# Performance work log

Hardware: AMD Instinct MI355X
Metric: run time of the kernel (lower is better)

The kernel has to match this reference:

```python
import jax, jax.numpy as jnp
import numpy as np
import math

B, T, C, H = 2, 2048, 1024, 16
HD = C // H  # head dim = 64

def setup_inputs() -> dict:
    key = jax.random.key(0)
    ks = jax.random.split(key, 5)
    s = 1.0 / math.sqrt(C)
    return {
        "x": jax.random.normal(ks[0], (B, T, C), jnp.float32),
        "Wq": jax.random.normal(ks[1], (C, C), jnp.float32) * s,
        "bq": jnp.zeros((C,), jnp.float32),
        "Wk": jax.random.normal(ks[2], (C, C), jnp.float32) * s,
        "bk": jnp.zeros((C,), jnp.float32),
        "Wv": jax.random.normal(ks[3], (C, C), jnp.float32) * s,
        "bv": jnp.zeros((C,), jnp.float32),
        "Wp": jax.random.normal(ks[4], (C, C), jnp.float32) * s,
        "bp": jnp.zeros((C,), jnp.float32),
    }

def reference(x, Wq, bq, Wk, bk, Wv, bv, Wp, bp):
    # project and split heads: [B,T,C] -> [B,H,T,HD]
    def heads(y):
        return y.reshape(B, T, H, HD).transpose(0, 2, 1, 3)
    q = heads(x @ Wq + bq)
    k = heads(x @ Wk + bk)
    v = heads(x @ Wv + bv)
    scale = 1.0 / math.sqrt(HD)
    att = jnp.einsum('bhqd,bhkd->bhqk', q, k) * scale  # [B,H,T,T]
    causal = jnp.tril(jnp.ones((T, T), bool))
    att = jnp.where(causal, att, -jnp.inf)
    att = jax.nn.softmax(att, axis=-1)  # attention_dropout p=0 -> identity
    y = jnp.einsum('bhqk,bhkd->bhqd', att, v)  # [B,H,T,HD]
    y = y.transpose(0, 2, 1, 3).reshape(B, T, C)
    return y @ Wp + bp  # residual_dropout p=0 -> identity
```

## Files before the change

### kernel.cpp

```cpp
#include <hip/hip_runtime.h>
#include <hip/hip_bf16.h>
#include <stdint.h>

typedef __bf16 bf16x8 __attribute__((ext_vector_type(8)));
typedef __bf16 bf16x4 __attribute__((ext_vector_type(4)));
typedef float  f32x4  __attribute__((ext_vector_type(4)));

#define MFMA16(a, b, c) __builtin_amdgcn_mfma_f32_16x16x32_bf16(a, b, c, 0, 0, 0)

#if __has_builtin(__builtin_amdgcn_exp2f)
#define EXP2(x) __builtin_amdgcn_exp2f(x)
#else
#define EXP2(x) exp2f(x)
#endif

__device__ __forceinline__ void ld16(void* lds, const void* g) {
    __builtin_amdgcn_global_load_lds(
        (const __attribute__((address_space(1))) void*)(uintptr_t)g,
        (__attribute__((address_space(3))) void*)(uint32_t)(uintptr_t)lds,
        16, 0, 0);
}

__global__ __launch_bounds__(1024) void prep_kernel(const float* __restrict__ x,
                                                    const float* __restrict__ W0,
                                                    const float* __restrict__ W1,
                                                    const float* __restrict__ W2,
                                                    const float* __restrict__ W3,
                                                    __bf16* __restrict__ wdst,
                                                    __bf16* __restrict__ xdst) {
    __shared__ __bf16 t[32][33];
    const int z = blockIdx.z;
    const int tx = threadIdx.x, ty = threadIdx.y;
    if (z == 4) {
        int blin = blockIdx.y * 32 + blockIdx.x;
        int i = (blin * 1024 + ty * 32 + tx) * 4;
        float4 v = *(const float4*)(x + i);
        xdst[i]     = (__bf16)v.x;
        xdst[i + 1] = (__bf16)v.y;
        xdst[i + 2] = (__bf16)v.z;
        xdst[i + 3] = (__bf16)v.w;
        return;
    }
    const float* W = (z == 0) ? W0 : (z == 1) ? W1 : (z == 2) ? W2 : W3;
    __bf16* D = wdst + (size_t)z * 1048576;
    t[ty][tx] = (__bf16)W[(size_t)(blockIdx.y * 32 + ty) * 1024 + blockIdx.x * 32 + tx];
    __syncthreads();
    D[(size_t)(blockIdx.x * 32 + ty) * 1024 + blockIdx.y * 32 + tx] = t[tx][ty];
}

__device__ __forceinline__ void gemm_mainloop(const __bf16* __restrict__ A,
                                              const __bf16* __restrict__ BT,
                                              int K, __bf16* As, __bf16* Bs,
                                              f32x4 acc[4][4]) {
    const int tid  = threadIdx.x;
    const int lane = tid & 63;
    const int wid  = tid >> 6;
    const int quad = lane >> 4;
    const int l16  = lane & 15;
    const int wm   = wid >> 1;
    const int wn   = wid & 1;

    const int srow = wid * 16 + (lane >> 2);
    const int scol = (lane & 3) * 8;
    const int sdst = wid * 512 + lane * 8;

    for (int k0 = 0; k0 < K; k0 += 32) {
        ld16(As + sdst,        A  + (size_t)srow        * K + k0 + scol);
        ld16(As + 2048 + sdst, A  + (size_t)(srow + 64) * K + k0 + scol);
        ld16(Bs + sdst,        BT + (size_t)srow        * K + k0 + scol);
        ld16(Bs + 2048 + sdst, BT + (size_t)(srow + 64) * K + k0 + scol);
        __syncthreads();
        bf16x8 af[4], bf[4];
#pragma unroll
        for (int mt = 0; mt < 4; mt++)
            af[mt] = *(const bf16x8*)(As + (wm * 64 + mt * 16 + l16) * 32 + quad * 8);
#pragma unroll
        for (int nt = 0; nt < 4; nt++)
            bf[nt] = *(const bf16x8*)(Bs + (wn * 64 + nt * 16 + l16) * 32 + quad * 8);
#pragma unroll
        for (int mt = 0; mt < 4; mt++)
#pragma unroll
            for (int nt = 0; nt < 4; nt++)
                acc[mt][nt] = MFMA16(af[mt], bf[nt], acc[mt][nt]);
        __syncthreads();
    }
}

__global__ __launch_bounds__(256) void qkv_gemm(const __bf16* __restrict__ X,
                                                const __bf16* __restrict__ WTb,
                                                const float* __restrict__ b0,
                                                const float* __restrict__ b1,
                                                const float* __restrict__ b2,
                                                __bf16* __restrict__ qk,
                                                __bf16* __restrict__ vt) {
    __shared__ __attribute__((aligned(16))) __bf16 As[4096];
    __shared__ __attribute__((aligned(16))) __bf16 Bs[4096];
    const int o  = blockIdx.x;
    const int g  = o & 7, r = o >> 3;
    const int mB = ((g >> 1) << 3) + (r & 7);
    const int nz = (g & 1) * 12 + (r >> 3);
    const int z  = nz >> 3;
    const int n  = nz & 7;
    const __bf16* BT   = WTb + (size_t)z * 1048576;
    const float* bias  = (z == 0) ? b0 : (z == 1) ? b1 : b2;
    const int m0 = mB * 128, n0 = n * 128;
    f32x4 acc[4][4];
    const f32x4 zz = {0.f, 0.f, 0.f, 0.f};
#pragma unroll
    for (int i = 0; i < 4; i++)
#pragma unroll
        for (int j = 0; j < 4; j++) acc[i][j] = zz;
    gemm_mainloop(X + (size_t)m0 * 1024, BT + (size_t)n0 * 1024, 1024, As, Bs, acc);

    const int lane = threadIdx.x & 63, wid = threadIdx.x >> 6;
    const int quad = lane >> 4, l16 = lane & 15, wm = wid >> 1, wn = wid & 1;
    if (z == 2) {
#pragma unroll
        for (int nt = 0; nt < 4; nt++) {
            int col = n0 + wn * 64 + nt * 16 + l16;
            float bv = bias[col];
            int h = col >> 6, hd = col & 63;
#pragma unroll
            for (int mt = 0; mt < 4; mt++) {
                int m = m0 + wm * 64 + mt * 16 + quad * 4;
                int b = m >> 11, tt = m & 2047;
                bf16x4 pk;
                pk.x = (__bf16)(acc[mt][nt].x + bv);
                pk.y = (__bf16)(acc[mt][nt].y + bv);
                pk.z = (__bf16)(acc[mt][nt].z + bv);
                pk.w = (__bf16)(acc[mt][nt].w + bv);
                *(bf16x4*)(vt + ((size_t)((b * 16 + h) * 64 + hd)) * 2048 + tt) = pk;
            }
        }
    } else {
        const float sq = (z == 0) ? 0.18033688011112042f : 1.0f;
        __bf16* dst = qk + (size_t)z * 4194304;
#pragma unroll
        for (int nt = 0; nt < 4; nt++) {
            int col = n0 + wn * 64 + nt * 16 + l16;
            float bv = bias[col];
            int h = col >> 6, hd = col & 63;
#pragma unroll
            for (int mt = 0; mt < 4; mt++) {
#pragma unroll
                for (int r4 = 0; r4 < 4; r4++) {
                    int m = m0 + wm * 64 + mt * 16 + quad * 4 + r4;
                    int b = m >> 11, tt = m & 2047;
                    float v = (acc[mt][nt][r4] + bv) * sq;
                    dst[((size_t)((b * 16 + h) * 2048 + tt)) * 64 + hd] = (__bf16)v;
                }
            }
        }
    }
}

__global__ __launch_bounds__(256) void proj_gemm(const __bf16* __restrict__ Yw,
                                                 const __bf16* __restrict__ WT,
                                                 const float* __restrict__ bias,
                                                 float* __restrict__ out) {
    __shared__ __attribute__((aligned(16))) __bf16 As[4096];
    __shared__ __attribute__((aligned(16))) __bf16 Bs[4096];
    const int o = blockIdx.x;
    const int g = o & 7, r = o >> 3;
    const int m0 = (g * 4 + (r & 3)) * 128;
    const int n0 = (r >> 2) * 128;
    f32x4 acc[4][4];
    const f32x4 zz = {0.f, 0.f, 0.f, 0.f};
#pragma unroll
    for (int i = 0; i < 4; i++)
#pragma unroll
        for (int j = 0; j < 4; j++) acc[i][j] = zz;
    gemm_mainloop(Yw + (size_t)m0 * 1024, WT + (size_t)n0 * 1024, 1024, As, Bs, acc);

    const int lane = threadIdx.x & 63, wid = threadIdx.x >> 6;
    const int quad = lane >> 4, l16 = lane & 15, wm = wid >> 1, wn = wid & 1;
#pragma unroll
    for (int nt = 0; nt < 4; nt++) {
        int col = n0 + wn * 64 + nt * 16 + l16;
        float bv = bias[col];
#pragma unroll
        for (int mt = 0; mt < 4; mt++) {
#pragma unroll
            for (int r4 = 0; r4 < 4; r4++) {
                int m = m0 + wm * 64 + mt * 16 + quad * 4 + r4;
                out[(size_t)m * 1024 + col] = acc[mt][nt][r4] + bv;
            }
        }
    }
}

__global__ __launch_bounds__(512, 1) void attn_kernel(const __bf16* __restrict__ Qg,
                                                      const __bf16* __restrict__ Kg,
                                                      const __bf16* __restrict__ Vtg,
                                                      __bf16* __restrict__ Y) {
    __shared__ __attribute__((aligned(16))) __bf16 Kb[2][128 * 64];
    __shared__ __attribute__((aligned(16))) __bf16 Vb[2][64 * 128];
    __shared__ __attribute__((aligned(16))) __bf16 Ps[8][16 * 136];
    __shared__ __attribute__((aligned(16))) float  Lw[8][16];

    const int tid  = threadIdx.x;
    const int lane = tid & 63;
    const int wid  = tid >> 6;
    const int quad = lane >> 4;
    const int l16  = lane & 15;
    const int bkid = blockIdx.x;
    const int head  = ((bkid & 7) << 2) + ((bkid >> 3) & 3);
    const int ipair = bkid >> 5;
    const size_t hbase = (size_t)head * (2048 * 64);
    const f32x4 zz = {0.f, 0.f, 0.f, 0.f};

    const int kr  = lane >> 3;
    const int kc8 = (lane & 7) ^ kr;
    const int vr  = lane >> 4;
    const int vl  = lane & 15;

#pragma unroll 1
    for (int itm = 0; itm < 2; itm++) {
        const int qi  = itm ? (15 - ipair) : ipair;
        const int ktl = qi;
        const int q0  = qi << 7;
        const int q0w = q0 + wid * 16;

        bf16x8 qf[2];
#pragma unroll
        for (int kk = 0; kk < 2; kk++)
            qf[kk] = *(const bf16x8*)(Qg + hbase +
                                      (size_t)(q0w + l16) * 64 + kk * 32 + quad * 8);

        f32x4 acc_o[4];
#pragma unroll
        for (int jj = 0; jj < 4; jj++) acc_o[jj] = zz;
        float l_s = 0.f;

        auto stage = [&](int bf, int key0) {
#pragma unroll
            for (int i = 0; i < 2; i++) {
                const int c = wid * 2 + i;
                ld16((char*)&Kb[bf][0] + c * 1024 + lane * 16,
                     Kg + hbase + (size_t)(key0 + c * 8 + kr) * 64 + kc8 * 8);
            }
#pragma unroll
            for (int i = 0; i < 2; i++) {
                const int c = wid * 2 + i;
                const int row = c * 4 + vr;
                const int vc  = vl ^ (row & 7);
                ld16((char*)&Vb[bf][0] + c * 1024 + lane * 16,
                     Vtg + hbase + (size_t)row * 2048 + key0 + vc * 8);
            }
        };

        stage(0, 0);
        __syncthreads();
        int buf = 0;

#pragma unroll 1
        for (int kt = 0; kt <= ktl; kt++) {
            if (kt < ktl) stage(buf ^ 1, (kt + 1) << 7);

            f32x4 accs[8];
#pragma unroll
            for (int mt = 0; mt < 8; mt++) accs[mt] = zz;
#pragma unroll
            for (int kk = 0; kk < 2; kk++) {
#pragma unroll
                for (int mt = 0; mt < 8; mt++) {
                    bf16x8 kf = *(const bf16x8*)(&Kb[buf][(mt * 16 + l16) * 64 +
                                                 (((kk * 4 + quad) ^ (l16 & 7)) << 3)]);
                    accs[mt] = MFMA16(kf, qf[kk], accs[mt]);
                }
            }

            if (kt == ktl) {
#pragma unroll
                for (int mt = 0; mt < 8; mt++) {
                    int q_g = wid * 16 + l16;
#pragma unroll
                    for (int r4 = 0; r4 < 4; r4++) {
                        int key_g = mt * 16 + quad * 4 + r4;
                        if (key_g > q_g) accs[mt][r4] = -1e30f;
                    }
                }
            }

            float s_s = 0.f;
#pragma unroll
            for (int mt = 0; mt < 8; mt++) {
                f32x4 pv;
                pv.x = EXP2(accs[mt].x);
                pv.y = EXP2(accs[mt].y);
                pv.z = EXP2(accs[mt].z);
                pv.w = EXP2(accs[mt].w);
                s_s += (pv.x + pv.y) + (pv.z + pv.w);
                bf16x4 pk;
                pk.x = (__bf16)pv.x; pk.y = (__bf16)pv.y;
                pk.z = (__bf16)pv.z; pk.w = (__bf16)pv.w;
                *(bf16x4*)(&Ps[wid][l16 * 136 + mt * 16 + quad * 4]) = pk;
            }
            {
                float t = s_s;
                t += __shfl_xor(t, 16);
                t += __shfl_xor(t, 32);
                l_s += t;
            }

#pragma unroll
            for (int kk = 0; kk < 4; kk++) {
                bf16x8 pf, vf[4];
                pf = *(const bf16x8*)(&Ps[wid][l16 * 136 + kk * 32 + quad * 8]);
#pragma unroll
                for (int nv = 0; nv < 4; nv++)
                    vf[nv] = *(const bf16x8*)(&Vb[buf][(nv * 16 + l16) * 128 +
                                              (((kk * 4 + quad) ^ (l16 & 7)) << 3)]);
#pragma unroll
                for (int nv = 0; nv < 4; nv++)
                    acc_o[nv] = MFMA16(pf, vf[nv], acc_o[nv]);
            }

            __syncthreads();
            buf ^= 1;
        }

        if (quad == 0) Lw[wid][l16] = l_s;
        float* Om = (float*)&Ps[wid][0];
#pragma unroll
        for (int nv = 0; nv < 4; nv++)
#pragma unroll
            for (int r4 = 0; r4 < 4; r4++)
                Om[(quad * 4 + r4) * 68 + nv * 16 + l16] = acc_o[nv][r4];
        __syncthreads();

        {
            const int q  = lane >> 2;
            const int d0 = (lane & 3) * 16;
            float li = 1.0f / Lw[wid][q];
            f32x4 s0 = *(const f32x4*)(&Om[q * 68 + d0]);
            f32x4 s1 = *(const f32x4*)(&Om[q * 68 + d0 + 4]);
            f32x4 s2 = *(const f32x4*)(&Om[q * 68 + d0 + 8]);
            f32x4 s3 = *(const f32x4*)(&Om[q * 68 + d0 + 12]);
            bf16x8 o0, o1;
            o0[0] = (__bf16)(s0.x * li); o0[1] = (__bf16)(s0.y * li);
            o0[2] = (__bf16)(s0.z * li); o0[3] = (__bf16)(s0.w * li);
            o0[4] = (__bf16)(s1.x * li); o0[5] = (__bf16)(s1.y * li);
            o0[6] = (__bf16)(s1.z * li); o0[7] = (__bf16)(s1.w * li);
            o1[0] = (__bf16)(s2.x * li); o1[1] = (__bf16)(s2.y * li);
            o1[2] = (__bf16)(s2.z * li); o1[3] = (__bf16)(s2.w * li);
            o1[4] = (__bf16)(s3.x * li); o1[5] = (__bf16)(s3.y * li);
            o1[6] = (__bf16)(s3.z * li); o1[7] = (__bf16)(s3.w * li);
            const int bb = head >> 4, hh = head & 15;
            __bf16* yp = Y + ((size_t)(bb * 2048 + q0w + q)) * 1024 + hh * 64 + d0;
            *(bf16x8*)(yp)     = o0;
            *(bf16x8*)(yp + 8) = o1;
        }
        __syncthreads();
    }
}

#define XB_OFF  0
#define WT_OFF  4194304
#define Q_OFF   8388608
#define K_OFF   12582912
#define VT_OFF  16777216
#define Y_OFF   0

extern "C" void kernel_launch(void* const* d_in, const int* in_sizes, int n_in,
                              void* d_out, int out_size, void* d_ws, size_t ws_size,
                              hipStream_t stream) {
    const float* x  = (const float*)d_in[0];
    const float* Wq = (const float*)d_in[1];
    const float* bq = (const float*)d_in[2];
    const float* Wk = (const float*)d_in[3];
    const float* bk = (const float*)d_in[4];
    const float* Wv = (const float*)d_in[5];
    const float* bv = (const float*)d_in[6];
    const float* Wp = (const float*)d_in[7];
    const float* bp = (const float*)d_in[8];
    __bf16* ws  = (__bf16*)d_ws;
    float*  out = (float*)d_out;
    if (ws_size < (size_t)41943040) return;

    prep_kernel<<<dim3(32, 32, 5), dim3(32, 32), 0, stream>>>(x, Wq, Wk, Wv, Wp,
                                                              ws + WT_OFF, ws + XB_OFF);
    qkv_gemm<<<dim3(768), 256, 0, stream>>>(ws + XB_OFF, ws + WT_OFF, bq, bk, bv,
                                            ws + Q_OFF, ws + VT_OFF);
    attn_kernel<<<dim3(256), 512, 0, stream>>>(ws + Q_OFF, ws + K_OFF, ws + VT_OFF,
                                               ws + Y_OFF);
    proj_gemm<<<dim3(256), 256, 0, stream>>>(ws + Y_OFF, ws + WT_OFF + 3 * 1048576, bp, out);
}
```

Baseline: 177.3 us.

## Widen GEMM K-tile to 64 with XOR-swizzled LDS and add MFMA priority hints

New measurement: 189.8 us. 1.07x slower.

```diff
diff --git a/kernel.cpp b/kernel.cpp
--- a/kernel.cpp
+++ b/kernel.cpp
@@ -60,28 +60,37 @@
     const int wm   = wid >> 1;
     const int wn   = wid & 1;
 
-    const int srow = wid * 16 + (lane >> 2);
-    const int scol = (lane & 3) * 8;
-    const int sdst = wid * 512 + lane * 8;
-
-    for (int k0 = 0; k0 < K; k0 += 32) {
-        ld16(As + sdst,        A  + (size_t)srow        * K + k0 + scol);
-        ld16(As + 2048 + sdst, A  + (size_t)(srow + 64) * K + k0 + scol);
-        ld16(Bs + sdst,        BT + (size_t)srow        * K + k0 + scol);
-        ld16(Bs + 2048 + sdst, BT + (size_t)(srow + 64) * K + k0 + scol);
+    const int lr = lane >> 3;
+    const int lc = (lane & 7) ^ lr;
+    const int l8 = l16 & 7;
+
+    for (int k0 = 0; k0 < K; k0 += 64) {
+#pragma unroll
+        for (int i = 0; i < 4; i++) {
+            const int r0 = wid * 32 + i * 8;
+            ld16((char*)As + r0 * 128 + lane * 16,
+                 A  + (size_t)(r0 + lr) * K + k0 + lc * 8);
+            ld16((char*)Bs + r0 * 128 + lane * 16,
+                 BT + (size_t)(r0 + lr) * K + k0 + lc * 8);
+        }
         __syncthreads();
-        bf16x8 af[4], bf[4];
-#pragma unroll
-        for (int mt = 0; mt < 4; mt++)
-            af[mt] = *(const bf16x8*)(As + (wm * 64 + mt * 16 + l16) * 32 + quad * 8);
-#pragma unroll
-        for (int nt = 0; nt < 4; nt++)
-            bf[nt] = *(const bf16x8*)(Bs + (wn * 64 + nt * 16 + l16) * 32 + quad * 8);
-#pragma unroll
-        for (int mt = 0; mt < 4; mt++)
+#pragma unroll
+        for (int kk = 0; kk < 2; kk++) {
+            bf16x8 af[4], bf[4];
+#pragma unroll
+            for (int mt = 0; mt < 4; mt++)
+                af[mt] = *(const bf16x8*)(As + (wm * 64 + mt * 16 + l16) * 64 +
+                                          (((kk * 4 + quad) ^ l8) << 3));
 #pragma unroll
             for (int nt = 0; nt < 4; nt++)
-                acc[mt][nt] = MFMA16(af[mt], bf[nt], acc[mt][nt]);
+                bf[nt] = *(const bf16x8*)(Bs + (wn * 64 + nt * 16 + l16) * 64 +
+                                          (((kk * 4 + quad) ^ l8) << 3));
+#pragma unroll
+            for (int mt = 0; mt < 4; mt++)
+#pragma unroll
+                for (int nt = 0; nt < 4; nt++)
+                    acc[mt][nt] = MFMA16(af[mt], bf[nt], acc[mt][nt]);
+        }
         __syncthreads();
     }
 }
@@ -93,8 +102,8 @@
                                                 const float* __restrict__ b2,
                                                 __bf16* __restrict__ qk,
                                                 __bf16* __restrict__ vt) {
-    __shared__ __attribute__((aligned(16))) __bf16 As[4096];
-    __shared__ __attribute__((aligned(16))) __bf16 Bs[4096];
+    __shared__ __attribute__((aligned(16))) __bf16 As[8192];
+    __shared__ __attribute__((aligned(16))) __bf16 Bs[8192];
     const int o  = blockIdx.x;
     const int g  = o & 7, r = o >> 3;
     const int mB = ((g >> 1) << 3) + (r & 7);
@@ -158,8 +167,8 @@
                                                  const __bf16* __restrict__ WT,
                                                  const float* __restrict__ bias,
                                                  float* __restrict__ out) {
-    __shared__ __attribute__((aligned(16))) __bf16 As[4096];
-    __shared__ __attribute__((aligned(16))) __bf16 Bs[4096];
+    __shared__ __attribute__((aligned(16))) __bf16 As[8192];
+    __shared__ __attribute__((aligned(16))) __bf16 Bs[8192];
     const int o = blockIdx.x;
     const int g = o & 7, r = o >> 3;
     const int m0 = (g * 4 + (r & 3)) * 128;
@@ -260,6 +269,7 @@
             f32x4 accs[8];
 #pragma unroll
             for (int mt = 0; mt < 8; mt++) accs[mt] = zz;
+            __builtin_amdgcn_s_setprio(1);
 #pragma unroll
             for (int kk = 0; kk < 2; kk++) {
 #pragma unroll
@@ -269,6 +279,7 @@
                     accs[mt] = MFMA16(kf, qf[kk], accs[mt]);
                 }
             }
+            __builtin_amdgcn_s_setprio(0);
 
             if (kt == ktl) {
 #pragma unroll
@@ -311,9 +322,11 @@
                 for (int nv = 0; nv < 4; nv++)
                     vf[nv] = *(const bf16x8*)(&Vb[buf][(nv * 16 + l16) * 128 +
                                               (((kk * 4 + quad) ^ (l16 & 7)) << 3)]);
+                __builtin_amdgcn_s_setprio(1);
 #pragma unroll
                 for (int nv = 0; nv < 4; nv++)
                     acc_o[nv] = MFMA16(pf, vf[nv], acc_o[nv]);
+                __builtin_amdgcn_s_setprio(0);
             }
 
             __syncthreads();
```

## Fuse prep, QKV GEMM, attention and projection into one persistent kernel

Applied to the files above, without the earlier changes.

Measured after the change: 278.3 us. 57.0% more time.

```diff
diff --git a/kernel.cpp b/kernel.cpp
--- a/kernel.cpp
+++ b/kernel.cpp
@@ -21,64 +21,51 @@
         16, 0, 0);
 }
 
-__global__ __launch_bounds__(1024) void prep_kernel(const float* __restrict__ x,
-                                                    const float* __restrict__ W0,
-                                                    const float* __restrict__ W1,
-                                                    const float* __restrict__ W2,
-                                                    const float* __restrict__ W3,
-                                                    __bf16* __restrict__ wdst,
-                                                    __bf16* __restrict__ xdst) {
-    __shared__ __bf16 t[32][33];
-    const int z = blockIdx.z;
-    const int tx = threadIdx.x, ty = threadIdx.y;
-    if (z == 4) {
-        int blin = blockIdx.y * 32 + blockIdx.x;
-        int i = (blin * 1024 + ty * 32 + tx) * 4;
-        float4 v = *(const float4*)(x + i);
-        xdst[i]     = (__bf16)v.x;
-        xdst[i + 1] = (__bf16)v.y;
-        xdst[i + 2] = (__bf16)v.z;
-        xdst[i + 3] = (__bf16)v.w;
-        return;
-    }
-    const float* W = (z == 0) ? W0 : (z == 1) ? W1 : (z == 2) ? W2 : W3;
-    __bf16* D = wdst + (size_t)z * 1048576;
-    t[ty][tx] = (__bf16)W[(size_t)(blockIdx.y * 32 + ty) * 1024 + blockIdx.x * 32 + tx];
+#define XB_OFF  0
+#define WT_OFF  4194304
+#define Q_OFF   8388608
+#define K_OFF   12582912
+#define VT_OFF  16777216
+#define Y_OFF   0
+
+__device__ __forceinline__ void gsync(unsigned* bar) {
     __syncthreads();
-    D[(size_t)(blockIdx.x * 32 + ty) * 1024 + blockIdx.y * 32 + tx] = t[tx][ty];
-}
-
-__device__ __forceinline__ void gemm_mainloop(const __bf16* __restrict__ A,
-                                              const __bf16* __restrict__ BT,
-                                              int K, __bf16* As, __bf16* Bs,
-                                              f32x4 acc[4][4]) {
+    if (threadIdx.x == 0) {
+        __threadfence();
+        atomicAdd(bar, 1u);
+        while (atomicAdd(bar, 0u) < 256u) { __builtin_amdgcn_s_sleep(8); }
+        __threadfence();
+    }
+    __syncthreads();
+}
+
+__device__ __forceinline__ void mainloop512(const __bf16* __restrict__ A,
+                                            const __bf16* __restrict__ BT,
+                                            __bf16* As, __bf16* Bs,
+                                            f32x4 acc[2][4]) {
     const int tid  = threadIdx.x;
     const int lane = tid & 63;
-    const int wid  = tid >> 6;
     const int quad = lane >> 4;
     const int l16  = lane & 15;
+    const int wid  = tid >> 6;
     const int wm   = wid >> 1;
     const int wn   = wid & 1;
-
-    const int srow = wid * 16 + (lane >> 2);
-    const int scol = (lane & 3) * 8;
-    const int sdst = wid * 512 + lane * 8;
-
-    for (int k0 = 0; k0 < K; k0 += 32) {
-        ld16(As + sdst,        A  + (size_t)srow        * K + k0 + scol);
-        ld16(As + 2048 + sdst, A  + (size_t)(srow + 64) * K + k0 + scol);
-        ld16(Bs + sdst,        BT + (size_t)srow        * K + k0 + scol);
-        ld16(Bs + 2048 + sdst, BT + (size_t)(srow + 64) * K + k0 + scol);
+    const int srow = tid >> 2;
+    const int scol = (tid & 3) * 8;
+
+    for (int k0 = 0; k0 < 1024; k0 += 32) {
+        ld16(As + tid * 8, A  + (size_t)srow * 1024 + k0 + scol);
+        ld16(Bs + tid * 8, BT + (size_t)srow * 1024 + k0 + scol);
         __syncthreads();
-        bf16x8 af[4], bf[4];
-#pragma unroll
-        for (int mt = 0; mt < 4; mt++)
-            af[mt] = *(const bf16x8*)(As + (wm * 64 + mt * 16 + l16) * 32 + quad * 8);
+        bf16x8 af[2], bf[4];
+#pragma unroll
+        for (int mt = 0; mt < 2; mt++)
+            af[mt] = *(const bf16x8*)(As + (wm * 32 + mt * 16 + l16) * 32 + quad * 8);
 #pragma unroll
         for (int nt = 0; nt < 4; nt++)
             bf[nt] = *(const bf16x8*)(Bs + (wn * 64 + nt * 16 + l16) * 32 + quad * 8);
 #pragma unroll
-        for (int mt = 0; mt < 4; mt++)
+        for (int mt = 0; mt < 2; mt++)
 #pragma unroll
             for (int nt = 0; nt < 4; nt++)
                 acc[mt][nt] = MFMA16(af[mt], bf[nt], acc[mt][nt]);
@@ -86,117 +73,14 @@
     }
 }
 
-__global__ __launch_bounds__(256) void qkv_gemm(const __bf16* __restrict__ X,
-                                                const __bf16* __restrict__ WTb,
-                                                const float* __restrict__ b0,
-                                                const float* __restrict__ b1,
-                                                const float* __restrict__ b2,
-                                                __bf16* __restrict__ qk,
-                                                __bf16* __restrict__ vt) {
-    __shared__ __attribute__((aligned(16))) __bf16 As[4096];
-    __shared__ __attribute__((aligned(16))) __bf16 Bs[4096];
-    const int o  = blockIdx.x;
-    const int g  = o & 7, r = o >> 3;
-    const int mB = ((g >> 1) << 3) + (r & 7);
-    const int nz = (g & 1) * 12 + (r >> 3);
-    const int z  = nz >> 3;
-    const int n  = nz & 7;
-    const __bf16* BT   = WTb + (size_t)z * 1048576;
-    const float* bias  = (z == 0) ? b0 : (z == 1) ? b1 : b2;
-    const int m0 = mB * 128, n0 = n * 128;
-    f32x4 acc[4][4];
-    const f32x4 zz = {0.f, 0.f, 0.f, 0.f};
-#pragma unroll
-    for (int i = 0; i < 4; i++)
-#pragma unroll
-        for (int j = 0; j < 4; j++) acc[i][j] = zz;
-    gemm_mainloop(X + (size_t)m0 * 1024, BT + (size_t)n0 * 1024, 1024, As, Bs, acc);
-
-    const int lane = threadIdx.x & 63, wid = threadIdx.x >> 6;
-    const int quad = lane >> 4, l16 = lane & 15, wm = wid >> 1, wn = wid & 1;
-    if (z == 2) {
-#pragma unroll
-        for (int nt = 0; nt < 4; nt++) {
-            int col = n0 + wn * 64 + nt * 16 + l16;
-            float bv = bias[col];
-            int h = col >> 6, hd = col & 63;
-#pragma unroll
-            for (int mt = 0; mt < 4; mt++) {
-                int m = m0 + wm * 64 + mt * 16 + quad * 4;
-                int b = m >> 11, tt = m & 2047;
-                bf16x4 pk;
-                pk.x = (__bf16)(acc[mt][nt].x + bv);
-                pk.y = (__bf16)(acc[mt][nt].y + bv);
-                pk.z = (__bf16)(acc[mt][nt].z + bv);
-                pk.w = (__bf16)(acc[mt][nt].w + bv);
-                *(bf16x4*)(vt + ((size_t)((b * 16 + h) * 64 + hd)) * 2048 + tt) = pk;
-            }
-        }
-    } else {
-        const float sq = (z == 0) ? 0.18033688011112042f : 1.0f;
-        __bf16* dst = qk + (size_t)z * 4194304;
-#pragma unroll
-        for (int nt = 0; nt < 4; nt++) {
-            int col = n0 + wn * 64 + nt * 16 + l16;
-            float bv = bias[col];
-            int h = col >> 6, hd = col & 63;
-#pragma unroll
-            for (int mt = 0; mt < 4; mt++) {
-#pragma unroll
-                for (int r4 = 0; r4 < 4; r4++) {
-                    int m = m0 + wm * 64 + mt * 16 + quad * 4 + r4;
-                    int b = m >> 11, tt = m & 2047;
-                    float v = (acc[mt][nt][r4] + bv) * sq;
-                    dst[((size_t)((b * 16 + h) * 2048 + tt)) * 64 + hd] = (__bf16)v;
-                }
-            }
-        }
-    }
-}
-
-__global__ __launch_bounds__(256) void proj_gemm(const __bf16* __restrict__ Yw,
-                                                 const __bf16* __restrict__ WT,
-                                                 const float* __restrict__ bias,
-                                                 float* __restrict__ out) {
-    __shared__ __attribute__((aligned(16))) __bf16 As[4096];
-    __shared__ __attribute__((aligned(16))) __bf16 Bs[4096];
-    const int o = blockIdx.x;
-    const int g = o & 7, r = o >> 3;
-    const int m0 = (g * 4 + (r & 3)) * 128;
-    const int n0 = (r >> 2) * 128;
-    f32x4 acc[4][4];
-    const f32x4 zz = {0.f, 0.f, 0.f, 0.f};
-#pragma unroll
-    for (int i = 0; i < 4; i++)
-#pragma unroll
-        for (int j = 0; j < 4; j++) acc[i][j] = zz;
-    gemm_mainloop(Yw + (size_t)m0 * 1024, WT + (size_t)n0 * 1024, 1024, As, Bs, acc);
-
-    const int lane = threadIdx.x & 63, wid = threadIdx.x >> 6;
-    const int quad = lane >> 4, l16 = lane & 15, wm = wid >> 1, wn = wid & 1;
-#pragma unroll
-    for (int nt = 0; nt < 4; nt++) {
-        int col = n0 + wn * 64 + nt * 16 + l16;
-        float bv = bias[col];
-#pragma unroll
-        for (int mt = 0; mt < 4; mt++) {
-#pragma unroll
-            for (int r4 = 0; r4 < 4; r4++) {
-                int m = m0 + wm * 64 + mt * 16 + quad * 4 + r4;
-                out[(size_t)m * 1024 + col] = acc[mt][nt][r4] + bv;
-            }
-        }
-    }
-}
-
-__global__ __launch_bounds__(512, 1) void attn_kernel(const __bf16* __restrict__ Qg,
-                                                      const __bf16* __restrict__ Kg,
-                                                      const __bf16* __restrict__ Vtg,
-                                                      __bf16* __restrict__ Y) {
-    __shared__ __attribute__((aligned(16))) __bf16 Kb[2][128 * 64];
-    __shared__ __attribute__((aligned(16))) __bf16 Vb[2][64 * 128];
-    __shared__ __attribute__((aligned(16))) __bf16 Ps[8][16 * 136];
-    __shared__ __attribute__((aligned(16))) float  Lw[8][16];
+__global__ __launch_bounds__(512, 1) void mega_kernel(
+        const float* __restrict__ x,
+        const float* __restrict__ Wq, const float* __restrict__ bq,
+        const float* __restrict__ Wk, const float* __restrict__ bk,
+        const float* __restrict__ Wv, const float* __restrict__ bv,
+        const float* __restrict__ Wp, const float* __restrict__ bp,
+        __bf16* ws, float* out, unsigned* bar) {
+    __shared__ __attribute__((aligned(16))) char smem[100864];
 
     const int tid  = threadIdx.x;
     const int lane = tid & 63;
@@ -204,163 +88,293 @@
     const int quad = lane >> 4;
     const int l16  = lane & 15;
     const int bkid = blockIdx.x;
-    const int head  = ((bkid & 7) << 2) + ((bkid >> 3) & 3);
-    const int ipair = bkid >> 5;
-    const size_t hbase = (size_t)head * (2048 * 64);
     const f32x4 zz = {0.f, 0.f, 0.f, 0.f};
 
-    const int kr  = lane >> 3;
-    const int kc8 = (lane & 7) ^ kr;
-    const int vr  = lane >> 4;
-    const int vl  = lane & 15;
+    {
+        __bf16* xb = ws + XB_OFF;
+        const int gtid = bkid * 512 + tid;
+#pragma unroll
+        for (int j = 0; j < 8; j++) {
+            int i = (gtid + j * 131072) * 4;
+            float4 v = *(const float4*)(x + i);
+            xb[i]     = (__bf16)v.x;
+            xb[i + 1] = (__bf16)v.y;
+            xb[i + 2] = (__bf16)v.z;
+            xb[i + 3] = (__bf16)v.w;
+        }
+        __bf16 (*t)[33] = (__bf16(*)[33])smem;
+        const int tx = tid & 31, ty = tid >> 5;
+        for (int tt = 0; tt < 16; tt++) {
+            const int tile = bkid * 16 + tt;
+            const int z = tile >> 10, rem = tile & 1023;
+            const int by = rem >> 5, bx = rem & 31;
+            const float* W = (z == 0) ? Wq : (z == 1) ? Wk : (z == 2) ? Wv : Wp;
+            __bf16* D = ws + WT_OFF + (size_t)z * 1048576;
+            t[ty][tx]      = (__bf16)W[(size_t)(by * 32 + ty) * 1024 + bx * 32 + tx];
+            t[ty + 16][tx] = (__bf16)W[(size_t)(by * 32 + ty + 16) * 1024 + bx * 32 + tx];
+            __syncthreads();
+            D[(size_t)(bx * 32 + ty) * 1024 + by * 32 + tx]      = t[tx][ty];
+            D[(size_t)(bx * 32 + ty + 16) * 1024 + by * 32 + tx] = t[tx][ty + 16];
+            __syncthreads();
+        }
+    }
+    gsync(&bar[0]);
+
+    {
+        __bf16* As = (__bf16*)smem;
+        __bf16* Bs = As + 4096;
+        const int g = bkid & 7, r0 = bkid >> 3;
+        const int wm = wid >> 1, wn = wid & 1;
+        for (int t3 = 0; t3 < 3; t3++) {
+            const int r  = r0 + t3 * 32;
+            const int mB = ((g >> 1) << 3) + (r & 7);
+            const int nz = (g & 1) * 12 + (r >> 3);
+            const int z  = nz >> 3;
+            const int n  = nz & 7;
+            const int m0 = mB * 128, n0 = n * 128;
+            const __bf16* BT  = ws + WT_OFF + (size_t)z * 1048576;
+            const float* bias = (z == 0) ? bq : (z == 1) ? bk : bv;
+            f32x4 acc[2][4];
+#pragma unroll
+            for (int i = 0; i < 2; i++)
+#pragma unroll
+                for (int j = 0; j < 4; j++) acc[i][j] = zz;
+            mainloop512(ws + XB_OFF + (size_t)m0 * 1024, BT + (size_t)n0 * 1024,
+                        As, Bs, acc);
+            if (z == 2) {
+                __bf16* vt = ws + VT_OFF;
+#pragma unroll
+                for (int nt = 0; nt < 4; nt++) {
+                    int col = n0 + wn * 64 + nt * 16 + l16;
+                    float bv = bias[col];
+                    int h = col >> 6, hd = col & 63;
+#pragma unroll
+                    for (int mt = 0; mt < 2; mt++) {
+                        int m = m0 + wm * 32 + mt * 16 + quad * 4;
+                        int b = m >> 11, tt = m & 2047;
+                        bf16x4 pk;
+                        pk.x = (__bf16)(acc[mt][nt].x + bv);
+                        pk.y = (__bf16)(acc[mt][nt].y + bv);
+                        pk.z = (__bf16)(acc[mt][nt].z + bv);
+                        pk.w = (__bf16)(acc[mt][nt].w + bv);
+                        *(bf16x4*)(vt + ((size_t)((b * 16 + h) * 64 + hd)) * 2048 + tt) = pk;
+                    }
+                }
+            } else {
+                const float sq = (z == 0) ? 0.18033688011112042f : 1.0f;
+                __bf16* dst = ws + Q_OFF + (size_t)z * 4194304;
+#pragma unroll
+                for (int nt = 0; nt < 4; nt++) {
+                    int col = n0 + wn * 64 + nt * 16 + l16;
+                    float bv = bias[col];
+                    int h = col >> 6, hd = col & 63;
+#pragma unroll
+                    for (int mt = 0; mt < 2; mt++) {
+#pragma unroll
+                        for (int r4 = 0; r4 < 4; r4++) {
+                            int m = m0 + wm * 32 + mt * 16 + quad * 4 + r4;
+                            int b = m >> 11, tt = m & 2047;
+                            float v = (acc[mt][nt][r4] + bv) * sq;
+                            dst[((size_t)((b * 16 + h) * 2048 + tt)) * 64 + hd] = (__bf16)v;
+                        }
+                    }
+                }
+            }
+        }
+    }
+    gsync(&bar[1]);
+
+    {
+        __bf16 (*Kb)[128 * 64] = (__bf16(*)[128 * 64])(smem);
+        __bf16 (*Vb)[64 * 128] = (__bf16(*)[64 * 128])(smem + 32768);
+        __bf16 (*Ps)[16 * 136] = (__bf16(*)[16 * 136])(smem + 65536);
+        float  (*Lw)[16]       = (float(*)[16])(smem + 100352);
+        const __bf16* Qg  = ws + Q_OFF;
+        const __bf16* Kg  = ws + K_OFF;
+        const __bf16* Vtg = ws + VT_OFF;
+        __bf16* Y = ws + Y_OFF;
+
+        const int head  = ((bkid & 7) << 2) + ((bkid >> 3) & 3);
+        const int ipair = bkid >> 5;
+        const size_t hbase = (size_t)head * (2048 * 64);
+
+        const int kr  = lane >> 3;
+        const int kc8 = (lane & 7) ^ kr;
+        const int vr  = lane >> 4;
+        const int vl  = lane & 15;
 
 #pragma unroll 1
-    for (int itm = 0; itm < 2; itm++) {
-        const int qi  = itm ? (15 - ipair) : ipair;
-        const int ktl = qi;
-        const int q0  = qi << 7;
-        const int q0w = q0 + wid * 16;
-
-        bf16x8 qf[2];
-#pragma unroll
-        for (int kk = 0; kk < 2; kk++)
-            qf[kk] = *(const bf16x8*)(Qg + hbase +
-                                      (size_t)(q0w + l16) * 64 + kk * 32 + quad * 8);
-
-        f32x4 acc_o[4];
-#pragma unroll
-        for (int jj = 0; jj < 4; jj++) acc_o[jj] = zz;
-        float l_s = 0.f;
-
-        auto stage = [&](int bf, int key0) {
-#pragma unroll
-            for (int i = 0; i < 2; i++) {
-                const int c = wid * 2 + i;
-                ld16((char*)&Kb[bf][0] + c * 1024 + lane * 16,
-                     Kg + hbase + (size_t)(key0 + c * 8 + kr) * 64 + kc8 * 8);
+        for (int itm = 0; itm < 2; itm++) {
+            const int qi  = itm ? (15 - ipair) : ipair;
+            const int ktl = qi;
+            const int q0  = qi << 7;
+            const int q0w = q0 + wid * 16;
+
+            bf16x8 qf[2];
+#pragma unroll
+            for (int kk = 0; kk < 2; kk++)
+                qf[kk] = *(const bf16x8*)(Qg + hbase +
+                                          (size_t)(q0w + l16) * 64 + kk * 32 + quad * 8);
+
+            f32x4 acc_o[4];
+#pragma unroll
+            for (int jj = 0; jj < 4; jj++) acc_o[jj] = zz;
+            float l_s = 0.f;
+
+            auto stage = [&](int bf, int key0) {
+#pragma unroll
+                for (int i = 0; i < 2; i++) {
+                    const int c = wid * 2 + i;
+                    ld16((char*)&Kb[bf][0] + c * 1024 + lane * 16,
+                         Kg + hbase + (size_t)(key0 + c * 8 + kr) * 64 + kc8 * 8);
+                }
+#pragma unroll
+                for (int i = 0; i < 2; i++) {
+                    const int c = wid * 2 + i;
+                    const int row = c * 4 + vr;
+                    const int vc  = vl ^ (row & 7);
+                    ld16((char*)&Vb[bf][0] + c * 1024 + lane * 16,
+                         Vtg + hbase + (size_t)row * 2048 + key0 + vc * 8);
+                }
+            };
+
+            stage(0, 0);
+            __syncthreads();
+            int buf = 0;
+
+#pragma unroll 1
+            for (int kt = 0; kt <= ktl; kt++) {
+                if (kt < ktl) stage(buf ^ 1, (kt + 1) << 7);
+
+                f32x4 accs[8];
+#pragma unroll
+                for (int mt = 0; mt < 8; mt++) accs[mt] = zz;
+#pragma unroll
+                for (int kk = 0; kk < 2; kk++) {
+#pragma unroll
+                    for (int mt = 0; mt < 8; mt++) {
+                        bf16x8 kf = *(const bf16x8*)(&Kb[buf][(mt * 16 + l16) * 64 +
+                                                     (((kk * 4 + quad) ^ (l16 & 7)) << 3)]);
+                        accs[mt] = MFMA16(kf, qf[kk], accs[mt]);
+                    }
+                }
+
+                if (kt == ktl) {
+#pragma unroll
+                    for (int mt = 0; mt < 8; mt++) {
+                        int q_g = wid * 16 + l16;
+#pragma unroll
+                        for (int r4 = 0; r4 < 4; r4++) {
+                            int key_g = mt * 16 + quad * 4 + r4;
+                            if (key_g > q_g) accs[mt][r4] = -1e30f;
+                        }
+                    }
+                }
+
+                float s_s = 0.f;
+#pragma unroll
+                for (int mt = 0; mt < 8; mt++) {
+                    f32x4 pv;
+                    pv.x = EXP2(accs[mt].x);
+                    pv.y = EXP2(accs[mt].y);
+                    pv.z = EXP2(accs[mt].z);
+                    pv.w = EXP2(accs[mt].w);
+                    s_s += (pv.x + pv.y) + (pv.z + pv.w);
+                    bf16x4 pk;
+                    pk.x = (__bf16)pv.x; pk.y = (__bf16)pv.y;
+                    pk.z = (__bf16)pv.z; pk.w = (__bf16)pv.w;
+                    *(bf16x4*)(&Ps[wid][l16 * 136 + mt * 16 + quad * 4]) = pk;
+                }
+                {
+                    float t = s_s;
+                    t += __shfl_xor(t, 16);
+                    t += __shfl_xor(t, 32);
+                    l_s += t;
+                }
+
+#pragma unroll
+                for (int kk = 0; kk < 4; kk++) {
+                    bf16x8 pf, vf[4];
+                    pf = *(const bf16x8*)(&Ps[wid][l16 * 136 + kk * 32 + quad * 8]);
+#pragma unroll
+                    for (int nv = 0; nv < 4; nv++)
+                        vf[nv] = *(const bf16x8*)(&Vb[buf][(nv * 16 + l16) * 128 +
+                                                  (((kk * 4 + quad) ^ (l16 & 7)) << 3)]);
+#pragma unroll
+                    for (int nv = 0; nv < 4; nv++)
+                        acc_o[nv] = MFMA16(pf, vf[nv], acc_o[nv]);
+                }
+
+                __syncthreads();
+                buf ^= 1;
             }
-#pragma unroll
-            for (int i = 0; i < 2; i++) {
-                const int c = wid * 2 + i;
-                const int row = c * 4 + vr;
-                const int vc  = vl ^ (row & 7);
-                ld16((char*)&Vb[bf][0] + c * 1024 + lane * 16,
-                     Vtg + hbase + (size_t)row * 2048 + key0 + vc * 8);
+
+            if (quad == 0) Lw[wid][l16] = l_s;
+            float* Om = (float*)&Ps[wid][0];
+#pragma unroll
+            for (int nv = 0; nv < 4; nv++)
+#pragma unroll
+                for (int r4 = 0; r4 < 4; r4++)
+                    Om[(quad * 4 + r4) * 68 + nv * 16 + l16] = acc_o[nv][r4];
+            __syncthreads();
+
+            {
+                const int q  = lane >> 2;
+                const int d0 = (lane & 3) * 16;
+                float li = 1.0f / Lw[wid][q];
+                f32x4 s0 = *(const f32x4*)(&Om[q * 68 + d0]);
+                f32x4 s1 = *(const f32x4*)(&Om[q * 68 + d0 + 4]);
+                f32x4 s2 = *(const f32x4*)(&Om[q * 68 + d0 + 8]);
+                f32x4 s3 = *(const f32x4*)(&Om[q * 68 + d0 + 12]);
+                bf16x8 o0, o1;
+                o0[0] = (__bf16)(s0.x * li); o0[1] = (__bf16)(s0.y * li);
+                o0[2] = (__bf16)(s0.z * li); o0[3] = (__bf16)(s0.w * li);
+                o0[4] = (__bf16)(s1.x * li); o0[5] = (__bf16)(s1.y * li);
+                o0[6] = (__bf16)(s1.z * li); o0[7] = (__bf16)(s1.w * li);
+                o1[0] = (__bf16)(s2.x * li); o1[1] = (__bf16)(s2.y * li);
+                o1[2] = (__bf16)(s2.z * li); o1[3] = (__bf16)(s2.w * li);
+                o1[4] = (__bf16)(s3.x * li); o1[5] = (__bf16)(s3.y * li);
+                o1[6] = (__bf16)(s3.z * li); o1[7] = (__bf16)(s3.w * li);
+                const int bb = head >> 4, hh = head & 15;
+                __bf16* yp = Y + ((size_t)(bb * 2048 + q0w + q)) * 1024 + hh * 64 + d0;
+                *(bf16x8*)(yp)     = o0;
+                *(bf16x8*)(yp + 8) = o1;
             }
-        };
-
-        stage(0, 0);
-        __syncthreads();
-        int buf = 0;
-
-#pragma unroll 1
-        for (int kt = 0; kt <= ktl; kt++) {
-            if (kt < ktl) stage(buf ^ 1, (kt + 1) << 7);
-
-            f32x4 accs[8];
-#pragma unroll
-            for (int mt = 0; mt < 8; mt++) accs[mt] = zz;
-#pragma unroll
-            for (int kk = 0; kk < 2; kk++) {
-#pragma unroll
-                for (int mt = 0; mt < 8; mt++) {
-                    bf16x8 kf = *(const bf16x8*)(&Kb[buf][(mt * 16 + l16) * 64 +
-                                                 (((kk * 4 + quad) ^ (l16 & 7)) << 3)]);
-                    accs[mt] = MFMA16(kf, qf[kk], accs[mt]);
+            __syncthreads();
+        }
+    }
+    gsync(&bar[2]);
+
+    {
+        __bf16* As = (__bf16*)smem;
+        __bf16* Bs = As + 4096;
+        const int g = bkid & 7, r = bkid >> 3;
+        const int m0 = (g * 4 + (r & 3)) * 128;
+        const int n0 = (r >> 2) * 128;
+        const int wm = wid >> 1, wn = wid & 1;
+        f32x4 acc[2][4];
+#pragma unroll
+        for (int i = 0; i < 2; i++)
+#pragma unroll
+            for (int j = 0; j < 4; j++) acc[i][j] = zz;
+        mainloop512(ws + Y_OFF + (size_t)m0 * 1024,
+                    ws + WT_OFF + (size_t)3 * 1048576 + (size_t)n0 * 1024,
+                    As, Bs, acc);
+#pragma unroll
+        for (int nt = 0; nt < 4; nt++) {
+            int col = n0 + wn * 64 + nt * 16 + l16;
+            float bv = bp[col];
+#pragma unroll
+            for (int mt = 0; mt < 2; mt++) {
+#pragma unroll
+                for (int r4 = 0; r4 < 4; r4++) {
+                    int m = m0 + wm * 32 + mt * 16 + quad * 4 + r4;
+                    out[(size_t)m * 1024 + col] = acc[mt][nt][r4] + bv;
                 }
             }
-
-            if (kt == ktl) {
-#pragma unroll
-                for (int mt = 0; mt < 8; mt++) {
-                    int q_g = wid * 16 + l16;
-#pragma unroll
-                    for (int r4 = 0; r4 < 4; r4++) {
-                        int key_g = mt * 16 + quad * 4 + r4;
-                        if (key_g > q_g) accs[mt][r4] = -1e30f;
-                    }
-                }
-            }
-
-            float s_s = 0.f;
-#pragma unroll
-            for (int mt = 0; mt < 8; mt++) {
-                f32x4 pv;
-                pv.x = EXP2(accs[mt].x);
-                pv.y = EXP2(accs[mt].y);
-                pv.z = EXP2(accs[mt].z);
-                pv.w = EXP2(accs[mt].w);
-                s_s += (pv.x + pv.y) + (pv.z + pv.w);
-                bf16x4 pk;
-                pk.x = (__bf16)pv.x; pk.y = (__bf16)pv.y;
-                pk.z = (__bf16)pv.z; pk.w = (__bf16)pv.w;
-                *(bf16x4*)(&Ps[wid][l16 * 136 + mt * 16 + quad * 4]) = pk;
-            }
-            {
-                float t = s_s;
-                t += __shfl_xor(t, 16);
-                t += __shfl_xor(t, 32);
-                l_s += t;
-            }
-
-#pragma unroll
-            for (int kk = 0; kk < 4; kk++) {
-                bf16x8 pf, vf[4];
-                pf = *(const bf16x8*)(&Ps[wid][l16 * 136 + kk * 32 + quad * 8]);
-#pragma unroll
-                for (int nv = 0; nv < 4; nv++)
-                    vf[nv] = *(const bf16x8*)(&Vb[buf][(nv * 16 + l16) * 128 +
-                                              (((kk * 4 + quad) ^ (l16 & 7)) << 3)]);
-#pragma unroll
-                for (int nv = 0; nv < 4; nv++)
-                    acc_o[nv] = MFMA16(pf, vf[nv], acc_o[nv]);
-            }
-
-            __syncthreads();
-            buf ^= 1;
-        }
-
-        if (quad == 0) Lw[wid][l16] = l_s;
-        float* Om = (float*)&Ps[wid][0];
-#pragma unroll
-        for (int nv = 0; nv < 4; nv++)
-#pragma unroll
-            for (int r4 = 0; r4 < 4; r4++)
-                Om[(quad * 4 + r4) * 68 + nv * 16 + l16] = acc_o[nv][r4];
-        __syncthreads();
-
-        {
-            const int q  = lane >> 2;
-            const int d0 = (lane & 3) * 16;
-            float li = 1.0f / Lw[wid][q];
-            f32x4 s0 = *(const f32x4*)(&Om[q * 68 + d0]);
-            f32x4 s1 = *(const f32x4*)(&Om[q * 68 + d0 + 4]);
-            f32x4 s2 = *(const f32x4*)(&Om[q * 68 + d0 + 8]);
-            f32x4 s3 = *(const f32x4*)(&Om[q * 68 + d0 + 12]);
-            bf16x8 o0, o1;
-            o0[0] = (__bf16)(s0.x * li); o0[1] = (__bf16)(s0.y * li);
-            o0[2] = (__bf16)(s0.z * li); o0[3] = (__bf16)(s0.w * li);
-            o0[4] = (__bf16)(s1.x * li); o0[5] = (__bf16)(s1.y * li);
-            o0[6] = (__bf16)(s1.z * li); o0[7] = (__bf16)(s1.w * li);
-            o1[0] = (__bf16)(s2.x * li); o1[1] = (__bf16)(s2.y * li);
-            o1[2] = (__bf16)(s2.z * li); o1[3] = (__bf16)(s2.w * li);
-            o1[4] = (__bf16)(s3.x * li); o1[5] = (__bf16)(s3.y * li);
-            o1[6] = (__bf16)(s3.z * li); o1[7] = (__bf16)(s3.w * li);
-            const int bb = head >> 4, hh = head & 15;
-            __bf16* yp = Y + ((size_t)(bb * 2048 + q0w + q)) * 1024 + hh * 64 + d0;
-            *(bf16x8*)(yp)     = o0;
-            *(bf16x8*)(yp + 8) = o1;
-        }
-        __syncthreads();
-    }
-}
-
-#define XB_OFF  0
-#define WT_OFF  4194304
-#define Q_OFF   8388608
-#define K_OFF   12582912
-#define VT_OFF  16777216
-#define Y_OFF   0
+        }
+    }
+}
 
 extern "C" void kernel_launch(void* const* d_in, const int* in_sizes, int n_in,
                               void* d_out, int out_size, void* d_ws, size_t ws_size,
@@ -378,11 +392,7 @@
     float*  out = (float*)d_out;
     if (ws_size < (size_t)41943040) return;
 
-    prep_kernel<<<dim3(32, 32, 5), dim3(32, 32), 0, stream>>>(x, Wq, Wk, Wv, Wp,
-                                                              ws + WT_OFF, ws + XB_OFF);
-    qkv_gemm<<<dim3(768), 256, 0, stream>>>(ws + XB_OFF, ws + WT_OFF, bq, bk, bv,
-                                            ws + Q_OFF, ws + VT_OFF);
-    attn_kernel<<<dim3(256), 512, 0, stream>>>(ws + Q_OFF, ws + K_OFF, ws + VT_OFF,
-                                               ws + Y_OFF);
-    proj_gemm<<<dim3(256), 256, 0, stream>>>(ws + Y_OFF, ws + WT_OFF + 3 * 1048576, bp, out);
-}
+    hipMemsetAsync(d_out, 0, 16, stream);
+    mega_kernel<<<dim3(256), dim3(512), 0, stream>>>(
+        x, Wq, bq, Wk, bk, Wv, bv, Wp, bp, ws, out, (unsigned*)d_out);
+}
```
